# Performance work log

Hardware: AMD Instinct MI355X
Metric: run time of the kernel (lower is better)

## Reference

```python
import jax, jax.numpy as jnp
import numpy as np
from jax import lax

B, T, D, H, S = 256, 512, 256, 512, 8


def setup_inputs() -> dict:
    key = jax.random.key(0)
    ks = jax.random.split(key, 8)
    bound = 1.0 / np.sqrt(H)  # torch LSTMCell/Linear default init scale
    u = lambda k_, shp: jax.random.uniform(k_, shp, jnp.float32, -bound, bound)
    _input = jax.random.normal(ks[0], (B, T, D), jnp.float32)
    h0 = jax.random.normal(ks[1], (B, H), jnp.float32)
    c0 = jax.random.normal(ks[2], (B, H), jnp.float32)
    W_ih = u(ks[3], (4 * H, D))
    W_hh = u(ks[4], (4 * H, H))
    b_ih = u(ks[5], (4 * H,))
    b_hh = u(ks[6], (4 * H,))
    W_lin = u(ks[7], (D, H))
    b_lin = jnp.zeros((D,), jnp.float32)
    # random skip weights per module logic: w1~Bern; w2=1 if w1==0 else Bern; first S steps (1,0)
    rng = np.random.default_rng(0)
    w1 = rng.integers(0, 2, T)
    w2 = np.where(w1 == 0, 1, rng.integers(0, 2, T))
    w1[:S] = 1
    w2[:S] = 0
    return {
        "_input": _input, "h0": h0, "c0": c0,
        "W_ih": W_ih, "W_hh": W_hh, "b_ih": b_ih, "b_hh": b_hh,
        "W_lin": W_lin, "b_lin": b_lin,
        "w1": jnp.asarray(w1, jnp.int32), "w2": jnp.asarray(w2, jnp.int32),
        "time_steps": T, "skip_size": S,
    }


def _lstm_cell(x, h, c, W_ih, W_hh, b_ih, b_hh):
    gates = x @ W_ih.T + b_ih + h @ W_hh.T + b_hh  # [B, 4H]
    i, f, g, o = jnp.split(gates, 4, axis=-1)
    i, f, o = jax.nn.sigmoid(i), jax.nn.sigmoid(f), jax.nn.sigmoid(o)
    c_new = f * c + i * jnp.tanh(g)
    h_new = o * jnp.tanh(c_new)
    return h_new, c_new


def reference(_input, h0, c0, W_ih, W_hh, b_ih, b_hh, W_lin, b_lin, w1, w2, time_steps, skip_size):
    # decoder-mode RSCN: feed previous linear(h) as next input
    buf_h = jnp.repeat(h0[None], skip_size, axis=0)  # FIFO queue as ring buffer [S,B,H]
    buf_c = jnp.repeat(c0[None], skip_size, axis=0)

    def step(carry, xs):
        h_feed, h, c, bh, bc = carry
        w1t, w2t, t = xs
        h_new, c_new = _lstm_cell(h_feed, h, c, W_ih, W_hh, b_ih, b_hh)
        pos = t % skip_size
        skip_h, skip_c = bh[pos], bc[pos]  # queue.get() (oldest)
        bh = bh.at[pos].set(h_new)          # queue.put(new)
        bc = bc.at[pos].set(c_new)
        a = w1t.astype(h_new.dtype)
        b = w2t.astype(h_new.dtype)
        norm = 1.0 / (a + b)
        comb_h = (a * h_new + b * jnp.tanh(skip_h)) * norm
        comb_c = (a * c_new + b * jnp.tanh(skip_c)) * norm
        out = comb_h @ W_lin.T + b_lin  # [B, D]
        return (out, comb_h, comb_c, bh, bc), out

    xs = (w1[:time_steps], w2[:time_steps], jnp.arange(time_steps))
    carry0 = (_input[:, 0, :], h0, c0, buf_h, buf_c)
    (_, h_fin, c_fin, _, _), outs = lax.scan(step, carry0, xs)
    return outs.transpose(1, 0, 2), h_fin, c_fin  # [B,T,D], final (h, c)
```

## Files before the change

### kernel.cpp

```cpp
#include <hip/hip_runtime.h>
#include <math.h>

#define BB 256
#define TT 512
#define DD 256
#define HH 512
#define SS 8
#define G4H 2048
#define BH (BB*HH)
#define OUT_BASE ((size_t)BB*TT*DD)
#define NGRP 16
#define GR 16
#define XSLOT_U32 4096
#define FSTRIDE 16

typedef _Float16 f16;
typedef __attribute__((ext_vector_type(8))) _Float16 f16x8;
typedef __attribute__((ext_vector_type(4))) float    f32x4;

__device__ __forceinline__ float sigm(float x) { return 1.f / (1.f + __expf(-x)); }
__device__ __forceinline__ float ftanh(float x) {
  x = fminf(15.f, fmaxf(-15.f, x));
  float e = __expf(-2.f * x);
  return (1.f - e) / (1.f + e);
}


__global__ __launch_bounds__(256) void prep_wbig16(
    const float* __restrict__ W_ih, const float* __restrict__ W_hh,
    const float* __restrict__ W_lin, f16* __restrict__ Wbig16)
{
  __shared__ float As[64][20];
  __shared__ float Bs[16][68];
  const int n0 = blockIdx.x * 64;
  const int j0 = blockIdx.y * 64;
  const int tid = threadIdx.x;
  const int tn = tid >> 4, tj = tid & 15;
  float acc[4][4] = {};
  for (int k0 = 0; k0 < DD; k0 += 16) {
    { int r = tid >> 2, c = (tid & 3) * 4;
      *(float4*)&As[r][c] = *(const float4*)&W_ih[(size_t)(n0 + r) * DD + k0 + c]; }
    { int r = tid >> 4, c = (tid & 15) * 4;
      *(float4*)&Bs[r][c] = *(const float4*)&W_lin[(size_t)(k0 + r) * HH + j0 + c]; }
    __syncthreads();
    #pragma unroll
    for (int k = 0; k < 16; ++k) {
      float a[4], bv[4];
      #pragma unroll
      for (int i = 0; i < 4; ++i) a[i] = As[tn*4+i][k];
      #pragma unroll
      for (int m = 0; m < 4; ++m) bv[m] = Bs[k][tj*4+m];
      #pragma unroll
      for (int i = 0; i < 4; ++i)
        #pragma unroll
        for (int m = 0; m < 4; ++m)
          acc[i][m] = fmaf(a[i], bv[m], acc[i][m]);
    }
    __syncthreads();
  }
  #pragma unroll
  for (int i = 0; i < 4; ++i) {
    int n = n0 + tn*4 + i;
    #pragma unroll
    for (int m = 0; m < 4; ++m) {
      int j = j0 + tj*4 + m;
      Wbig16[(size_t)n*HH + j] = (f16)(acc[i][m] + W_hh[(size_t)n*HH + j]);
    }
  }
}

__global__ void prep_bias(const float* __restrict__ b_ih, const float* __restrict__ b_hh,
                          const float* __restrict__ W_ih, const float* __restrict__ b_lin,
                          float* __restrict__ bias0, float* __restrict__ bias1)
{
  int n = blockIdx.x * 256 + threadIdx.x;
  float s = b_ih[n] + b_hh[n];
  float d = 0.f;
  for (int k = 0; k < DD; ++k) d = fmaf(W_ih[(size_t)n*DD + k], b_lin[k], d);
  bias0[n] = s;
  bias1[n] = s + d;
}

#define NIH (G4H*DD)
#define NHH (G4H*HH)
__global__ void prep_cvtw(const float* __restrict__ W_ih, const float* __restrict__ W_hh,
                          const float* __restrict__ W_lin,
                          f16* __restrict__ Wih16, f16* __restrict__ Whh16,
                          f16* __restrict__ Wlin16)
{
  int e = blockIdx.x * 256 + threadIdx.x;
  if (e < NIH) Wih16[e] = (f16)W_ih[e];
  else if (e < NIH + NHH) Whh16[e - NIH] = (f16)W_hh[e - NIH];
  else Wlin16[e - NIH - NHH] = (f16)W_lin[e - NIH - NHH];
}

__global__ void prep_init(const float* __restrict__ x0, const float* __restrict__ h0,
                          const float* __restrict__ c0,
                          const int* __restrict__ w1, const int* __restrict__ w2,
                          float* __restrict__ bh, float* __restrict__ bc,
                          f16* __restrict__ x0hi, f16* __restrict__ x0lo,
                          f16* __restrict__ h0hi, f16* __restrict__ h0lo,
                          float4* __restrict__ stepc,
                          int* __restrict__ flags)
{
  int e = blockIdx.x * 256 + threadIdx.x;
  int r = e & (BH - 1);
  bh[e] = h0[r];
  bc[e] = c0[r];
  if (e < BH) {
    float v = h0[e];
    f16 hi = (f16)v;
    h0hi[e] = hi;
    h0lo[e] = (f16)(v - (float)hi);
  }
  if (e < BB*DD) {
    int b = e >> 8, d = e & 255;
    float v = x0[(size_t)b*(TT*DD) + d];
    f16 hi = (f16)v;
    x0hi[e] = hi;
    x0lo[e] = (f16)(v - (float)hi);
  }
  if (e < TT) {
    float a1 = (float)w1[e], a2 = (float)w2[e];
    stepc[e] = make_float4(a1, a2, 1.f / (a1 + a2), 0.f);
  }
  if (e < 4096) flags[e] = 0;
}


__device__ __forceinline__ void stageG(const unsigned* __restrict__ Xs,
                                       f16* lds, int tid) {
  const int lane = tid & 63;
  const int wv = tid >> 6;
  #pragma unroll
  for (int i = 0; i < 2; ++i) {
    int r = wv * 2 + i;
    const char* src = (const char*)Xs + (size_t)r * 1024 +
                      (size_t)((lane ^ r) & 63) * 16;
    __builtin_amdgcn_global_load_lds(
        (const __attribute__((address_space(1))) void*)src,
        (__attribute__((address_space(3))) void*)((char*)lds + r * 1024),
        16, 0, 0x11 );
  }
}

__device__ __forceinline__ void gemm16(const f16x8 (&wA)[16], const f16x8 (&wB)[16],
                                       const f16* lds, int lane,
                                       f32x4& acc0, f32x4& acc1) {
  const int r  = lane & 15;
  const int kc = lane >> 4;
  const int rb = r * 1024;
  #pragma unroll
  for (int ks = 0; ks < 16; ++ks) {
    int u = ks * 4 + kc;
    f16x8 a = *(const f16x8*)((const char*)lds + rb + ((u ^ r) << 4));
    acc0 = __builtin_amdgcn_mfma_f32_16x16x32_f16(a, wA[ks], acc0, 0, 0, 0);
    acc1 = __builtin_amdgcn_mfma_f32_16x16x32_f16(a, wB[ks], acc1, 0, 0, 0);
  }
}

__global__ __launch_bounds__(512, 2) void lstm_persist(
    const f16* __restrict__ x0hi, const f16* __restrict__ x0lo,
    const f16* __restrict__ h0hi, const f16* __restrict__ h0lo,
    const float* __restrict__ c0,
    const f16* __restrict__ Wih16, const f16* __restrict__ Whh16,
    const f16* __restrict__ Wbig16, const f16* __restrict__ Wlin16,
    const float* __restrict__ bias0, const float* __restrict__ bias1,
    const float* __restrict__ b_lin,
    const float4* __restrict__ stepc,
    unsigned* __restrict__ X,
    float* __restrict__ bh, float* __restrict__ bc,
    int* __restrict__ flags,
    float* __restrict__ outp)
{
  __shared__ f16 LdsA[8192];
  __shared__ float gbuf[4096];

  const int tid  = threadIdx.x;
  const int lane = tid & 63;
  const int wv   = tid >> 6;
  const int bid  = blockIdx.x;
  const bool isG = bid < 128;
  const int grp  = isG ? (bid & 15) : (bid - 128);
  const int role = bid >> 4;
  const int b0   = grp * GR;
  const int r16  = lane & 15;
  const int kc   = lane >> 4;
  const int ksel = kc * 8;

  int* gflag = flags + grp * 9 * FSTRIDE;

  int rowA, rowB;
  const f16* wsrc;
  if (isG) {
    rowA = (wv & 3) * 512 + role * 64 + (wv >> 2) * 32 + r16;
    rowB = rowA + 16;
    wsrc = Wbig16;
  } else {
    rowA = wv * 32 + r16;
    rowB = rowA + 16;
    wsrc = Wlin16;
  }
  f16x8 wA[16], wB[16];
  #pragma unroll
  for (int ks = 0; ks < 16; ++ks) {
    wA[ks] = *(const f16x8*)(wsrc + (size_t)rowA * HH + ks * 32 + ksel);
    wB[ks] = *(const f16x8*)(wsrc + (size_t)rowB * HH + ks * 32 + ksel);
  }

  if (isG) {
    int   eidx[2];
    float creg[2];
    const int jl = tid & 63;
    const int jg = role * 64 + jl;
    const float bI = bias1[jg],        bF = bias1[512 + jg];
    const float bG = bias1[1024 + jg], bO = bias1[1536 + jg];
    #pragma unroll
    for (int i = 0; i < 2; ++i) {
      int c = i * 512 + tid;
      int bl = c >> 6;
      eidx[i] = (b0 + bl) * HH + jg;
      creg[i] = c0[eidx[i]];
    }

    for (int t = 0; t < TT; ++t) {
      if (t > 0) {
        if (lane < 8) {
          while (__hip_atomic_load(&gflag[lane * FSTRIDE], __ATOMIC_RELAXED,
                                   __HIP_MEMORY_SCOPE_AGENT) < t) {}
        } else if (lane == 8 && t >= 4) {
          while (__hip_atomic_load(&gflag[8 * FSTRIDE], __ATOMIC_RELAXED,
                                   __HIP_MEMORY_SCOPE_AGENT) < t - 3) {}
        }
        stageG(X + (size_t)(((t - 1) & 3) * NGRP + grp) * XSLOT_U32, LdsA, tid);
      }

      const float4 sc = stepc[t];
      const int pos = t & (SS - 1);
      float shv[2], scv[2];
      #pragma unroll
      for (int i = 0; i < 2; ++i) {
        int bx = pos * BH + eidx[i];
        shv[i] = bh[bx];
        scv[i] = bc[bx];
      }

      f32x4 acc0, acc1;
      #pragma unroll
      for (int i = 0; i < 4; ++i) { acc0[i] = 0.f; acc1[i] = 0.f; }
      if (t == 0) {
        const f16* arh = x0hi + (size_t)(b0 + r16) * DD;
        const f16* arl = x0lo + (size_t)(b0 + r16) * DD;
        const f16* wap = Wih16 + (size_t)rowA * DD;
        const f16* wbp = Wih16 + (size_t)rowB * DD;
        #pragma unroll
        for (int ks = 0; ks < 8; ++ks) {
          int ko = ks * 32 + ksel;
          f16x8 wa = *(const f16x8*)(wap + ko);
          f16x8 wb = *(const f16x8*)(wbp + ko);
          f16x8 ah = *(const f16x8*)(arh + ko);
          f16x8 al = *(const f16x8*)(arl + ko);
          acc0 = __builtin_amdgcn_mfma_f32_16x16x32_f16(ah, wa, acc0, 0, 0, 0);
          acc1 = __builtin_amdgcn_mfma_f32_16x16x32_f16(ah, wb, acc1, 0, 0, 0);
          acc0 = __builtin_amdgcn_mfma_f32_16x16x32_f16(al, wa, acc0, 0, 0, 0);
          acc1 = __builtin_amdgcn_mfma_f32_16x16x32_f16(al, wb, acc1, 0, 0, 0);
        }
        const f16* brh = h0hi + (size_t)(b0 + r16) * HH;
        const f16* brl = h0lo + (size_t)(b0 + r16) * HH;
        const f16* qap = Whh16 + (size_t)rowA * HH;
        const f16* qbp = Whh16 + (size_t)rowB * HH;
        #pragma unroll
        for (int ks = 0; ks < 16; ++ks) {
          int ko = ks * 32 + ksel;
          f16x8 wa = *(const f16x8*)(qap + ko);
          f16x8 wb = *(const f16x8*)(qbp + ko);
          f16x8 ah = *(const f16x8*)(brh + ko);
          f16x8 al = *(const f16x8*)(brl + ko);
          acc0 = __builtin_amdgcn_mfma_f32_16x16x32_f16(ah, wa, acc0, 0, 0, 0);
          acc1 = __builtin_amdgcn_mfma_f32_16x16x32_f16(ah, wb, acc1, 0, 0, 0);
          acc0 = __builtin_amdgcn_mfma_f32_16x16x32_f16(al, wa, acc0, 0, 0, 0);
          acc1 = __builtin_amdgcn_mfma_f32_16x16x32_f16(al, wb, acc1, 0, 0, 0);
        }
      } else {
        __syncthreads();
        gemm16(wA, wB, LdsA, lane, acc0, acc1);
      }

      {
        const int g4 = wv & 3, jh = wv >> 2;
        #pragma unroll
        for (int rg = 0; rg < 4; ++rg) {
          int m  = kc * 4 + rg;
          int j0 = jh * 32 + r16;
          int cs0 = (j0      + 16 * kc) & 63;
          int cs1 = (j0 + 16 + 16 * kc) & 63;
          gbuf[g4 * 1024 + m * 64 + cs0] = acc0[rg];
          gbuf[g4 * 1024 + m * 64 + cs1] = acc1[rg];
        }
      }
      __syncthreads();

      const float a1 = sc.x, a2 = sc.y, nrm = sc.z;
      float baI = bI, baF = bF, baG = bG, baO = bO;
      if (t == 0) {
        baI = bias0[jg];        baF = bias0[512 + jg];
        baG = bias0[1024 + jg]; baO = bias0[1536 + jg];
      }
      unsigned* Xw = X + (size_t)((t & 3) * NGRP + grp) * XSLOT_U32;
      float hnv[2], cnv[2], chv[2];
      #pragma unroll
      for (int i = 0; i < 2; ++i) {
        int c = i * 512 + tid;
        int bl = c >> 6;
        int jj = c & 63;
        int gofs = bl * 64 + ((jj + 16 * (bl >> 2)) & 63);
        float pi = gbuf[gofs]        + baI;
        float pf = gbuf[1024 + gofs] + baF;
        float pg = gbuf[2048 + gofs] + baG;
        float po = gbuf[3072 + gofs] + baO;
        float i_ = sigm(pi), f_ = sigm(pf), o_ = sigm(po), g_ = ftanh(pg);
        float cnew = fmaf(f_, creg[i], i_ * g_);
        float hnew = o_ * ftanh(cnew);
        float ch = (a1 * hnew + a2 * ftanh(shv[i])) * nrm;
        hnv[i] = hnew; cnv[i] = cnew; chv[i] = ch;
        f16 hv = (f16)ch;
        unsigned hb = (unsigned)*(const unsigned short*)&hv;
        unsigned part = (unsigned)__shfl_xor((int)hb, 1);
        if ((tid & 1) == 0)
          __hip_atomic_store(&Xw[bl * 256 + (jg >> 1)], hb | (part << 16),
                             __ATOMIC_RELAXED, __HIP_MEMORY_SCOPE_AGENT);
      }
      __syncthreads();
      if (tid == 0)
        __hip_atomic_store(&gflag[role * FSTRIDE], t + 1, __ATOMIC_RELAXED,
                           __HIP_MEMORY_SCOPE_AGENT);

      #pragma unroll
      for (int i = 0; i < 2; ++i) {
        float cc = (a1 * cnv[i] + a2 * ftanh(scv[i])) * nrm;
        creg[i] = cc;
        int bx = pos * BH + eidx[i];
        bh[bx] = hnv[i];
        bc[bx] = cnv[i];
        if (t == TT - 1) {
          __builtin_nontemporal_store(chv[i], &outp[OUT_BASE + eidx[i]]);
          __builtin_nontemporal_store(cc,     &outp[OUT_BASE + BH + eidx[i]]);
        }
      }
    }
  } else {
    const float bld0 = b_lin[rowA];
    const float bld1 = b_lin[rowB];
    for (int s = 0; s < TT; ++s) {
      if (lane < 8) {
        while (__hip_atomic_load(&gflag[lane * FSTRIDE], __ATOMIC_RELAXED,
                                 __HIP_MEMORY_SCOPE_AGENT) < s + 1) {}
      }
      stageG(X + (size_t)((s & 3) * NGRP + grp) * XSLOT_U32, LdsA, tid);
      __syncthreads();
      if (tid == 0)
        __hip_atomic_store(&gflag[8 * FSTRIDE], s + 1, __ATOMIC_RELAXED,
                           __HIP_MEMORY_SCOPE_AGENT);
      f32x4 acc0, acc1;
      #pragma unroll
      for (int i = 0; i < 4; ++i) { acc0[i] = 0.f; acc1[i] = 0.f; }
      gemm16(wA, wB, LdsA, lane, acc0, acc1);
      const size_t tbase = (size_t)s * DD + wv * 32 + r16;
      #pragma unroll
      for (int rg = 0; rg < 4; ++rg) {
        int m = kc * 4 + rg;
        __builtin_nontemporal_store(acc0[rg] + bld0,
                                    &outp[(size_t)(b0 + m) * (TT*DD) + tbase]);
        __builtin_nontemporal_store(acc1[rg] + bld1,
                                    &outp[(size_t)(b0 + m) * (TT*DD) + tbase + 16]);
      }
      __syncthreads();
    }
  }
}


extern "C" void kernel_launch(void* const* d_in, const int* in_sizes, int n_in,
                              void* d_out, int out_size, void* d_ws, size_t ws_size,
                              hipStream_t stream)
{
  const float* x0    = (const float*)d_in[0];
  const float* h0    = (const float*)d_in[1];
  const float* c0    = (const float*)d_in[2];
  const float* W_ih  = (const float*)d_in[3];
  const float* W_hh  = (const float*)d_in[4];
  const float* b_ih  = (const float*)d_in[5];
  const float* b_hh  = (const float*)d_in[6];
  const float* W_lin = (const float*)d_in[7];
  const float* b_lin = (const float*)d_in[8];
  const int*   w1    = (const int*)d_in[9];
  const int*   w2    = (const int*)d_in[10];

  char* p = (char*)d_ws;
  f16* Wbig16 = (f16*)p;            p += (size_t)G4H*HH*2;
  f16* Wih16  = (f16*)p;            p += (size_t)G4H*DD*2;
  f16* Whh16  = (f16*)p;            p += (size_t)G4H*HH*2;
  f16* Wlin16 = (f16*)p;            p += (size_t)DD*HH*2;
  f16* x0hi   = (f16*)p;            p += (size_t)BB*DD*2;
  f16* x0lo   = (f16*)p;            p += (size_t)BB*DD*2;
  f16* h0hi   = (f16*)p;            p += (size_t)BH*2;
  f16* h0lo   = (f16*)p;            p += (size_t)BH*2;
  unsigned* X = (unsigned*)p;       p += (size_t)4*NGRP*XSLOT_U32*4;
  float* bh   = (float*)p;          p += (size_t)SS*BH*4;
  float* bc   = (float*)p;          p += (size_t)SS*BH*4;
  float* bias0= (float*)p;          p += G4H*4;
  float* bias1= (float*)p;          p += G4H*4;
  float4* stepc = (float4*)p;       p += (size_t)TT*16;
  int*  flags = (int*)p;            p += 4096*4;
  float* outp = (float*)d_out;

  hipLaunchKernelGGL(prep_wbig16, dim3(32, 8), dim3(256), 0, stream,
                     W_ih, W_hh, W_lin, Wbig16);
  hipLaunchKernelGGL(prep_bias, dim3(8), dim3(256), 0, stream,
                     b_ih, b_hh, W_ih, b_lin, bias0, bias1);
  hipLaunchKernelGGL(prep_cvtw, dim3(6656), dim3(256), 0, stream,
                     W_ih, W_hh, W_lin, Wih16, Whh16, Wlin16);
  hipLaunchKernelGGL(prep_init, dim3(4096), dim3(256), 0, stream,
                     x0, h0, c0, w1, w2, bh, bc, x0hi, x0lo, h0hi, h0lo, stepc, flags);

  hipLaunchKernelGGL(lstm_persist, dim3(128 + NGRP), dim3(512), 0, stream,
                     x0hi, x0lo, h0hi, h0lo, c0, Wih16, Whh16, Wbig16, Wlin16,
                     bias0, bias1, b_lin, stepc, X, bh, bc, flags, outp);
}
```

Measured before the change: 1.601 ms.

## Per-wave stripe staging so each wave waits only on its producer's flag

Changes the X exchange layout so each producer role writes a contiguous 2 KB stripe with an 8-wide swizzle. Each wave now polls only the flag of the role that produces its stripe and stages just that stripe, instead of all waves waiting on all eight flags. The wait-and-stage also moves after the ring-buffer loads so those global reads overlap the spin. The GEMM LDS addressing is updated to the new swizzle, and a barrier is added on the t==0 path. This cuts global synchronization latency per step, but correctness depends on the new layout and barrier placement matching between producers and consumers.

```diff
diff --git a/kernel.cpp b/kernel.cpp
--- a/kernel.cpp
+++ b/kernel.cpp
@@ -128,18 +128,17 @@
 }
 
 
-__device__ __forceinline__ void stageG(const unsigned* __restrict__ Xs,
-                                       f16* lds, int tid) {
-  const int lane = tid & 63;
-  const int wv = tid >> 6;
+__device__ __forceinline__ void stage_stripe(const unsigned* __restrict__ Xs,
+                                             int w, f16* lds, int lane) {
   #pragma unroll
   for (int i = 0; i < 2; ++i) {
-    int r = wv * 2 + i;
-    const char* src = (const char*)Xs + (size_t)r * 1024 +
-                      (size_t)((lane ^ r) & 63) * 16;
+    int q = i * 64 + lane;
+    int row = q >> 3, u = q & 7;
+    const char* src = (const char*)Xs + w * 2048 + row * 128 +
+                      ((u ^ (row & 7)) << 4);
     __builtin_amdgcn_global_load_lds(
         (const __attribute__((address_space(1))) void*)src,
-        (__attribute__((address_space(3))) void*)((char*)lds + r * 1024),
+        (__attribute__((address_space(3))) void*)((char*)lds + w * 2048 + i * 1024),
         16, 0, 0x11 );
   }
 }
@@ -149,11 +148,12 @@
                                        f32x4& acc0, f32x4& acc1) {
   const int r  = lane & 15;
   const int kc = lane >> 4;
-  const int rb = r * 1024;
   #pragma unroll
   for (int ks = 0; ks < 16; ++ks) {
-    int u = ks * 4 + kc;
-    f16x8 a = *(const f16x8*)((const char*)lds + rb + ((u ^ r) << 4));
+    int role_k = ks >> 1;
+    int u = ((ks & 1) << 2) + kc;
+    int off = role_k * 2048 + r * 128 + ((u ^ (r & 7)) << 4);
+    f16x8 a = *(const f16x8*)((const char*)lds + off);
     acc0 = __builtin_amdgcn_mfma_f32_16x16x32_f16(a, wA[ks], acc0, 0, 0, 0);
     acc1 = __builtin_amdgcn_mfma_f32_16x16x32_f16(a, wB[ks], acc1, 0, 0, 0);
   }
@@ -224,17 +224,6 @@
     }
 
     for (int t = 0; t < TT; ++t) {
-      if (t > 0) {
-        if (lane < 8) {
-          while (__hip_atomic_load(&gflag[lane * FSTRIDE], __ATOMIC_RELAXED,
-                                   __HIP_MEMORY_SCOPE_AGENT) < t) {}
-        } else if (lane == 8 && t >= 4) {
-          while (__hip_atomic_load(&gflag[8 * FSTRIDE], __ATOMIC_RELAXED,
-                                   __HIP_MEMORY_SCOPE_AGENT) < t - 3) {}
-        }
-        stageG(X + (size_t)(((t - 1) & 3) * NGRP + grp) * XSLOT_U32, LdsA, tid);
-      }
-
       const float4 sc = stepc[t];
       const int pos = t & (SS - 1);
       float shv[2], scv[2];
@@ -243,6 +232,18 @@
         int bx = pos * BH + eidx[i];
         shv[i] = bh[bx];
         scv[i] = bc[bx];
+      }
+
+      if (t > 0) {
+        if (lane == 0) {
+          while (__hip_atomic_load(&gflag[wv * FSTRIDE], __ATOMIC_RELAXED,
+                                   __HIP_MEMORY_SCOPE_AGENT) < t) {}
+        } else if (wv == 0 && lane == 1 && t >= 4) {
+          while (__hip_atomic_load(&gflag[8 * FSTRIDE], __ATOMIC_RELAXED,
+                                   __HIP_MEMORY_SCOPE_AGENT) < t - 3) {}
+        }
+        stage_stripe(X + (size_t)(((t - 1) & 3) * NGRP + grp) * XSLOT_U32,
+                     wv, LdsA, lane);
       }
 
       f32x4 acc0, acc1;
@@ -281,6 +282,7 @@
           acc0 = __builtin_amdgcn_mfma_f32_16x16x32_f16(al, wa, acc0, 0, 0, 0);
           acc1 = __builtin_amdgcn_mfma_f32_16x16x32_f16(al, wb, acc1, 0, 0, 0);
         }
+        __syncthreads();
       } else {
         __syncthreads();
         gemm16(wA, wB, LdsA, lane, acc0, acc1);
@@ -327,7 +329,7 @@
         unsigned hb = (unsigned)*(const unsigned short*)&hv;
         unsigned part = (unsigned)__shfl_xor((int)hb, 1);
         if ((tid & 1) == 0)
-          __hip_atomic_store(&Xw[bl * 256 + (jg >> 1)], hb | (part << 16),
+          __hip_atomic_store(&Xw[role * 512 + bl * 32 + (jl >> 1)], hb | (part << 16),
                              __ATOMIC_RELAXED, __HIP_MEMORY_SCOPE_AGENT);
       }
       __syncthreads();
@@ -352,11 +354,11 @@
     const float bld0 = b_lin[rowA];
     const float bld1 = b_lin[rowB];
     for (int s = 0; s < TT; ++s) {
-      if (lane < 8) {
-        while (__hip_atomic_load(&gflag[lane * FSTRIDE], __ATOMIC_RELAXED,
+      if (lane == 0) {
+        while (__hip_atomic_load(&gflag[wv * FSTRIDE], __ATOMIC_RELAXED,
                                  __HIP_MEMORY_SCOPE_AGENT) < s + 1) {}
       }
-      stageG(X + (size_t)((s & 3) * NGRP + grp) * XSLOT_U32, LdsA, tid);
+      stage_stripe(X + (size_t)((s & 3) * NGRP + grp) * XSLOT_U32, wv, LdsA, lane);
       __syncthreads();
       if (tid == 0)
         __hip_atomic_store(&gflag[8 * FSTRIDE], s + 1, __ATOMIC_RELAXED,
```

New measurement: 1.425 ms. -11.0%, faster.
